# Kernel tuning notes

Hardware: AMD Instinct MI355X
Metric: run time of the kernel (lower is better)

## Reference

```python
import jax, jax.numpy as jnp
import numpy as np

HIDDEN = 1024
N_HEADS = 16
HEAD_DIM = HIDDEN // N_HEADS
MAX_DIST = 50
B, S = 2, 2048


def setup_inputs() -> dict:
    key = jax.random.key(0)
    ks = jax.random.split(key, 12)
    s = 1.0 / np.sqrt(HIDDEN)
    return {
        "hidden_states": jax.random.normal(ks[0], (B, S, HIDDEN), dtype=jnp.float32),
        "dist_matrix": jax.random.randint(ks[1], (B, S, S), 0, 60, dtype=jnp.int32),
        "idf_scores": jax.random.uniform(ks[2], (B, S), dtype=jnp.float32),
        "attention_mask": jnp.ones((B, S), dtype=jnp.int32),
        "Wq": jax.random.normal(ks[3], (HIDDEN, HIDDEN), dtype=jnp.float32) * s,
        "bq": jnp.zeros((HIDDEN,), dtype=jnp.float32),
        "Wk": jax.random.normal(ks[4], (HIDDEN, HIDDEN), dtype=jnp.float32) * s,
        "bk": jnp.zeros((HIDDEN,), dtype=jnp.float32),
        "Wv": jax.random.normal(ks[5], (HIDDEN, HIDDEN), dtype=jnp.float32) * s,
        "bv": jnp.zeros((HIDDEN,), dtype=jnp.float32),
        "Wo": jax.random.normal(ks[6], (HIDDEN, HIDDEN), dtype=jnp.float32) * s,
        "bo": jnp.zeros((HIDDEN,), dtype=jnp.float32),
        "struct_emb": jax.random.normal(ks[7], (MAX_DIST + 1, N_HEADS), dtype=jnp.float32) * 0.02,
        "rarity_weight": jnp.full((1,), 0.1, dtype=jnp.float32),
    }


def reference(hidden_states, dist_matrix, idf_scores, attention_mask,
              Wq, bq, Wk, bk, Wv, bv, Wo, bo, struct_emb, rarity_weight):
    b, s, _ = hidden_states.shape
    scale = 1.0 / np.sqrt(HEAD_DIM)

    def split_heads(x):  # [b,s,H] -> [b,h,s,d]
        return x.reshape(b, s, N_HEADS, HEAD_DIM).transpose(0, 2, 1, 3)

    Q = split_heads(hidden_states @ Wq.T + bq)
    K = split_heads(hidden_states @ Wk.T + bk)
    V = split_heads(hidden_states @ Wv.T + bv)

    scores = jnp.einsum('bhqd,bhkd->bhqk', Q, K) * scale

    # structural bias: gather per-head bias by clamped pairwise distance
    dist_c = jnp.clip(dist_matrix, 0, MAX_DIST)
    scores = scores + struct_emb[dist_c].transpose(0, 3, 1, 2)  # [b,h,q,k]

    # rarity bias: idf_i broadcasts over keys, idf_j over queries (as in torch code)
    rarity = rarity_weight[0] * (idf_scores[:, None, None, :] + idf_scores[:, None, :, None])
    scores = scores + rarity

    # mask: [b,1,1,s] over key axis
    mask = attention_mask[:, None, None, :]
    scores = jnp.where(mask == 0, -jnp.inf, scores)

    attn = jax.nn.softmax(scores, axis=-1)
    out = jnp.einsum('bhqk,bhkd->bhqd', attn, V)
    out = out.transpose(0, 2, 1, 3).reshape(b, s, HIDDEN)
    out = out @ Wo.T + bo
    return out, attn
```

## Files before the change

### kernel.cpp

```cpp
#include <hip/hip_runtime.h>
#include <math.h>

#define S 2048
#define HID 1024
#define NH 16
#define HD 64
#define BH 32

typedef __attribute__((ext_vector_type(8))) short bf16x8;
typedef __attribute__((ext_vector_type(4))) float f32x4;
typedef __attribute__((ext_vector_type(8))) unsigned short ush8;
typedef unsigned short u16;

__device__ __forceinline__ u16 f2bf(float f) {
    unsigned u = __float_as_uint(f);
    u += 0x7fffu + ((u >> 16) & 1u);
    return (u16)(u >> 16);
}
__device__ __forceinline__ float bf2f(u16 h) {
    return __uint_as_float(((unsigned)h) << 16);
}

__global__ __launch_bounds__(256)
void split_all(const float* __restrict__ X,  const float* __restrict__ Wq,
               const float* __restrict__ Wk, const float* __restrict__ Wv,
               const float* __restrict__ Wo,
               u16* __restrict__ Xh,  u16* __restrict__ Xl,
               u16* __restrict__ Wqh, u16* __restrict__ Wql,
               u16* __restrict__ Wkh, u16* __restrict__ Wkl,
               u16* __restrict__ Wvh, u16* __restrict__ Wvl,
               u16* __restrict__ Woh, u16* __restrict__ Wol)
{
    size_t i = (size_t)blockIdx.x * 256 + threadIdx.x;
    const float* s; u16* h; u16* l; size_t o;
    if (i < (size_t)(1u << 20)) { s = X; h = Xh; l = Xl; o = i; }
    else {
        size_t j = i - (1u << 20);
        int wsel = (int)(j >> 18); o = j & ((1u << 18) - 1);
        s = wsel == 0 ? Wq  : wsel == 1 ? Wk  : wsel == 2 ? Wv  : Wo;
        h = wsel == 0 ? Wqh : wsel == 1 ? Wkh : wsel == 2 ? Wvh : Woh;
        l = wsel == 0 ? Wql : wsel == 1 ? Wkl : wsel == 2 ? Wvl : Wol;
    }
    float4 v = ((const float4*)s)[o];
    ushort4 hv, lv;
#define SP(c, k) { unsigned u = __float_as_uint(v.c);                      \
                   unsigned hb = u & 0xffff0000u;                          \
                   float d = v.c - __uint_as_float(hb);                    \
                   hv.k = (u16)(u >> 16);                                  \
                   lv.k = (u16)(__float_as_uint(d) >> 16); }
    SP(x, x) SP(y, y) SP(z, z) SP(w, w)
#undef SP
    ((ushort4*)h)[o] = hv;
    ((ushort4*)l)[o] = lv;
}

__global__ __launch_bounds__(256)
void qkv_mfma(const u16* __restrict__ Xh, const u16* __restrict__ Xl,
              const u16* __restrict__ Wh_q, const u16* __restrict__ Wl_q,
              const u16* __restrict__ Wh_k, const u16* __restrict__ Wl_k,
              const u16* __restrict__ Wh_v, const u16* __restrict__ Wl_v,
              const float* __restrict__ bq_, const float* __restrict__ bk_,
              const float* __restrict__ bv_,
              u16* __restrict__ Qb, u16* __restrict__ Kb, u16* __restrict__ Vb)
{
    const int z = blockIdx.z;
    const u16* __restrict__ Wh = z == 0 ? Wh_q : (z == 1 ? Wh_k : Wh_v);
    const u16* __restrict__ Wl = z == 0 ? Wl_q : (z == 1 ? Wl_k : Wl_v);
    const float* __restrict__ bias = z == 0 ? bq_ : (z == 1 ? bk_ : bv_);
    u16* __restrict__ Ob = z == 0 ? Qb : (z == 1 ? Kb : Vb);

    __shared__ u16 Ah[128 * 40], Al[128 * 40], Bh[128 * 40], Bl[128 * 40];
    const int t = threadIdx.x;
    const int m0 = blockIdx.y * 128, n0 = blockIdx.x * 128;
    const int srow = t >> 1, scol = (t & 1) * 16;
    const int lane = t & 63, w = t >> 6, wm = w >> 1, wn = w & 1;
    const int lr = lane & 15, lg = lane >> 4;

    f32x4 acc[4][4] = {{{0.f, 0.f, 0.f, 0.f}}};
    for (int k0 = 0; k0 < HID; k0 += 32) {
        size_t ao = (size_t)(m0 + srow) * HID + k0 + scol;
        size_t bo = (size_t)(n0 + srow) * HID + k0 + scol;
        ush8 a0 = *(const ush8*)(Xh + ao), a1 = *(const ush8*)(Xh + ao + 8);
        ush8 a2 = *(const ush8*)(Xl + ao), a3 = *(const ush8*)(Xl + ao + 8);
        ush8 b0 = *(const ush8*)(Wh + bo), b1 = *(const ush8*)(Wh + bo + 8);
        ush8 b2 = *(const ush8*)(Wl + bo), b3 = *(const ush8*)(Wl + bo + 8);
        __syncthreads();
        *(ush8*)&Ah[srow * 40 + scol] = a0; *(ush8*)&Ah[srow * 40 + scol + 8] = a1;
        *(ush8*)&Al[srow * 40 + scol] = a2; *(ush8*)&Al[srow * 40 + scol + 8] = a3;
        *(ush8*)&Bh[srow * 40 + scol] = b0; *(ush8*)&Bh[srow * 40 + scol + 8] = b1;
        *(ush8*)&Bl[srow * 40 + scol] = b2; *(ush8*)&Bl[srow * 40 + scol + 8] = b3;
        __syncthreads();
        bf16x8 fbh[4], fbl[4];
#pragma unroll
        for (int ni = 0; ni < 4; ++ni) {
            fbh[ni] = *(const bf16x8*)&Bh[(wn * 64 + ni * 16 + lr) * 40 + lg * 8];
            fbl[ni] = *(const bf16x8*)&Bl[(wn * 64 + ni * 16 + lr) * 40 + lg * 8];
        }
#pragma unroll
        for (int mi = 0; mi < 4; ++mi) {
            bf16x8 fah = *(const bf16x8*)&Ah[(wm * 64 + mi * 16 + lr) * 40 + lg * 8];
            bf16x8 fal = *(const bf16x8*)&Al[(wm * 64 + mi * 16 + lr) * 40 + lg * 8];
#pragma unroll
            for (int ni = 0; ni < 4; ++ni) {
                f32x4 c = acc[mi][ni];
                c = __builtin_amdgcn_mfma_f32_16x16x32_bf16(fah, fbh[ni], c, 0, 0, 0);
                c = __builtin_amdgcn_mfma_f32_16x16x32_bf16(fah, fbl[ni], c, 0, 0, 0);
                c = __builtin_amdgcn_mfma_f32_16x16x32_bf16(fal, fbh[ni], c, 0, 0, 0);
                acc[mi][ni] = c;
            }
        }
    }
    const int hh = blockIdx.x * 2 + wn;
    float bv4[4];
#pragma unroll
    for (int ni = 0; ni < 4; ++ni) bv4[ni] = bias[n0 + wn * 64 + ni * 16 + lr];
#pragma unroll
    for (int mi = 0; mi < 4; ++mi)
#pragma unroll
        for (int r = 0; r < 4; ++r) {
            int m = m0 + wm * 64 + mi * 16 + lg * 4 + r;
            int b = m >> 11, s = m & 2047;
#pragma unroll
            for (int ni = 0; ni < 4; ++ni) {
                float v = acc[mi][ni][r] + bv4[ni];
                Ob[((size_t)(b * NH + hh) * S + s) * HD + ni * 16 + lr] = f2bf(v);
            }
        }
}

__global__ __launch_bounds__(256)
void out_mfma(const u16* __restrict__ Xh, const u16* __restrict__ Xl,
              const u16* __restrict__ Wh, const u16* __restrict__ Wl,
              const float* __restrict__ bo_, float* __restrict__ Y)
{
    __shared__ u16 Ah[128 * 40], Al[128 * 40], Bh[128 * 40], Bl[128 * 40];
    const int t = threadIdx.x;
    const int m0 = blockIdx.y * 128, n0 = blockIdx.x * 128;
    const int srow = t >> 1, scol = (t & 1) * 16;
    const int lane = t & 63, w = t >> 6, wm = w >> 1, wn = w & 1;
    const int lr = lane & 15, lg = lane >> 4;

    f32x4 acc[4][4] = {{{0.f, 0.f, 0.f, 0.f}}};
    for (int k0 = 0; k0 < HID; k0 += 32) {
        size_t ao = (size_t)(m0 + srow) * HID + k0 + scol;
        size_t bo = (size_t)(n0 + srow) * HID + k0 + scol;
        ush8 a0 = *(const ush8*)(Xh + ao), a1 = *(const ush8*)(Xh + ao + 8);
        ush8 a2 = *(const ush8*)(Xl + ao), a3 = *(const ush8*)(Xl + ao + 8);
        ush8 b0 = *(const ush8*)(Wh + bo), b1 = *(const ush8*)(Wh + bo + 8);
        ush8 b2 = *(const ush8*)(Wl + bo), b3 = *(const ush8*)(Wl + bo + 8);
        __syncthreads();
        *(ush8*)&Ah[srow * 40 + scol] = a0; *(ush8*)&Ah[srow * 40 + scol + 8] = a1;
        *(ush8*)&Al[srow * 40 + scol] = a2; *(ush8*)&Al[srow * 40 + scol + 8] = a3;
        *(ush8*)&Bh[srow * 40 + scol] = b0; *(ush8*)&Bh[srow * 40 + scol + 8] = b1;
        *(ush8*)&Bl[srow * 40 + scol] = b2; *(ush8*)&Bl[srow * 40 + scol + 8] = b3;
        __syncthreads();
        bf16x8 fbh[4], fbl[4];
#pragma unroll
        for (int ni = 0; ni < 4; ++ni) {
            fbh[ni] = *(const bf16x8*)&Bh[(wn * 64 + ni * 16 + lr) * 40 + lg * 8];
            fbl[ni] = *(const bf16x8*)&Bl[(wn * 64 + ni * 16 + lr) * 40 + lg * 8];
        }
#pragma unroll
        for (int mi = 0; mi < 4; ++mi) {
            bf16x8 fah = *(const bf16x8*)&Ah[(wm * 64 + mi * 16 + lr) * 40 + lg * 8];
            bf16x8 fal = *(const bf16x8*)&Al[(wm * 64 + mi * 16 + lr) * 40 + lg * 8];
#pragma unroll
            for (int ni = 0; ni < 4; ++ni) {
                f32x4 c = acc[mi][ni];
                c = __builtin_amdgcn_mfma_f32_16x16x32_bf16(fah, fbh[ni], c, 0, 0, 0);
                c = __builtin_amdgcn_mfma_f32_16x16x32_bf16(fah, fbl[ni], c, 0, 0, 0);
                c = __builtin_amdgcn_mfma_f32_16x16x32_bf16(fal, fbh[ni], c, 0, 0, 0);
                acc[mi][ni] = c;
            }
        }
    }
    float bv4[4];
#pragma unroll
    for (int ni = 0; ni < 4; ++ni) bv4[ni] = bo_[n0 + wn * 64 + ni * 16 + lr];
#pragma unroll
    for (int mi = 0; mi < 4; ++mi)
#pragma unroll
        for (int r = 0; r < 4; ++r) {
            int m = m0 + wm * 64 + mi * 16 + lg * 4 + r;
#pragma unroll
            for (int ni = 0; ni < 4; ++ni)
                Y[(size_t)m * HID + n0 + wn * 64 + ni * 16 + lr] =
                    acc[mi][ni][r] + bv4[ni];
        }
}

__global__ __launch_bounds__(512)
void attn_pv(const u16* __restrict__ Qb, const u16* __restrict__ Kb,
             const u16* __restrict__ Vb,
             const int* __restrict__ dist, const float* __restrict__ idf,
             const int* __restrict__ amask, const float* __restrict__ semb,
             const float* __restrict__ rw,
             float* __restrict__ attn, u16* __restrict__ OHh, u16* __restrict__ OHl)
{
    __shared__ u16 QPs[128 * 72];
    __shared__ u16 Ks[64 * 72];
    __shared__ u16 Vts[64 * 72];
    __shared__ float SeH[51];

    const int n = blockIdx.x;
    const int xcd = n & 7, rest = n >> 3;
    const int h = rest & 15;
    const int pair = xcd * 4 + (rest >> 4);
    const int b = pair >> 4, qt = pair & 15;
    const int bh = b * NH + h, q0 = qt * 128;

    const int t = threadIdx.x, lane = t & 63, w = t >> 6;
    const int lr = lane & 15, lg = lane >> 4;

    if (t < 51) SeH[t] = semb[t * NH + h];
    {
        int r = t >> 2, c = (t & 3) * 16;
        const u16* qrow = Qb + ((size_t)bh * S + q0 + r) * HD + c;
        *(ush8*)&QPs[r * 72 + c]     = *(const ush8*)qrow;
        *(ush8*)&QPs[r * 72 + c + 8] = *(const ush8*)(qrow + 8);
    }
    __syncthreads();

    bf16x8 qa0 = *(const bf16x8*)&QPs[(w * 16 + lr) * 72 + lg * 8];
    bf16x8 qa1 = *(const bf16x8*)&QPs[(w * 16 + lr) * 72 + 32 + lg * 8];

    const float rwv = rw[0];
    float idqv[4];
#pragma unroll
    for (int r = 0; r < 4; ++r)
        idqv[r] = idf[b * S + q0 + w * 16 + lg * 4 + r];

    float M[4]    = {-INFINITY, -INFINITY, -INFINITY, -INFINITY};
    float Ssum[4] = {0.f, 0.f, 0.f, 0.f};

    for (int k0 = 0; k0 < S; k0 += 64) {
        __syncthreads();
        *(ush8*)&Ks[(t >> 3) * 72 + (t & 7) * 8] =
            *(const ush8*)(Kb + ((size_t)bh * S + k0 + (t >> 3)) * HD + (t & 7) * 8);
        __syncthreads();

        f32x4 c4[4];
#pragma unroll
        for (int ni = 0; ni < 4; ++ni) {
            bf16x8 kf0 = *(const bf16x8*)&Ks[(ni * 16 + lr) * 72 + lg * 8];
            bf16x8 kf1 = *(const bf16x8*)&Ks[(ni * 16 + lr) * 72 + 32 + lg * 8];
            f32x4 c = {0.f, 0.f, 0.f, 0.f};
            c = __builtin_amdgcn_mfma_f32_16x16x32_bf16(qa0, kf0, c, 0, 0, 0);
            c = __builtin_amdgcn_mfma_f32_16x16x32_bf16(qa1, kf1, c, 0, 0, 0);
            c4[ni] = c;
        }

        float idk[4]; int mk[4];
#pragma unroll
        for (int ni = 0; ni < 4; ++ni) {
            int k = k0 + ni * 16 + lr;
            idk[ni] = idf[b * S + k];
            mk[ni]  = amask[b * S + k];
        }
#pragma unroll
        for (int r = 0; r < 4; ++r) {
            const int q = q0 + w * 16 + lg * 4 + r;
            const int* drow = dist + ((size_t)b * S + q) * S + k0;
            float sc[4];
#pragma unroll
            for (int ni = 0; ni < 4; ++ni) {
                int dc = drow[ni * 16 + lr];
                dc = dc < 0 ? 0 : (dc > 50 ? 50 : dc);
                float v = c4[ni][r] * 0.125f + SeH[dc] + rwv * (idqv[r] + idk[ni]);
                if (mk[ni] == 0) v = -INFINITY;
                sc[ni] = v;
            }
            float m = fmaxf(fmaxf(sc[0], sc[1]), fmaxf(sc[2], sc[3]));
#pragma unroll
            for (int off = 1; off < 16; off <<= 1) m = fmaxf(m, __shfl_xor(m, off));
            if (m > -INFINITY) {
                float s = 0.f;
#pragma unroll
                for (int ni = 0; ni < 4; ++ni) s += __expf(sc[ni] - m);
#pragma unroll
                for (int off = 1; off < 16; off <<= 1) s += __shfl_xor(s, off);
                if (m > M[r]) {
                    Ssum[r] = Ssum[r] * __expf(M[r] - m) + s;
                    M[r] = m;
                } else {
                    Ssum[r] += s * __expf(m - M[r]);
                }
            }
        }
    }
    float Iv[4];
#pragma unroll
    for (int r = 0; r < 4; ++r) Iv[r] = 1.0f / Ssum[r];

    f32x4 oacc[4] = {{0.f, 0.f, 0.f, 0.f}};

    for (int k0 = 0; k0 < S; k0 += 64) {
        __syncthreads();
        *(ush8*)&Ks[(t >> 3) * 72 + (t & 7) * 8] =
            *(const ush8*)(Kb + ((size_t)bh * S + k0 + (t >> 3)) * HD + (t & 7) * 8);
        {
            ush8 v0 = *(const ush8*)(Vb + ((size_t)bh * S + k0 + lane) * HD + w * 8);
#pragma unroll
            for (int j = 0; j < 8; ++j)
                Vts[(w * 8 + j) * 72 + lane] = ((const u16*)&v0)[j];
        }
        __syncthreads();

        f32x4 c4[4];
#pragma unroll
        for (int ni = 0; ni < 4; ++ni) {
            bf16x8 kf0 = *(const bf16x8*)&Ks[(ni * 16 + lr) * 72 + lg * 8];
            bf16x8 kf1 = *(const bf16x8*)&Ks[(ni * 16 + lr) * 72 + 32 + lg * 8];
            f32x4 c = {0.f, 0.f, 0.f, 0.f};
            c = __builtin_amdgcn_mfma_f32_16x16x32_bf16(qa0, kf0, c, 0, 0, 0);
            c = __builtin_amdgcn_mfma_f32_16x16x32_bf16(qa1, kf1, c, 0, 0, 0);
            c4[ni] = c;
        }

        float idk[4]; int mk[4];
#pragma unroll
        for (int ni = 0; ni < 4; ++ni) {
            int k = k0 + ni * 16 + lr;
            idk[ni] = idf[b * S + k];
            mk[ni]  = amask[b * S + k];
        }
#pragma unroll
        for (int r = 0; r < 4; ++r) {
            const int q = q0 + w * 16 + lg * 4 + r;
            const int* drow = dist + ((size_t)b * S + q) * S + k0;
            float* arow = attn + ((size_t)bh * S + q) * S + k0;
#pragma unroll
            for (int ni = 0; ni < 4; ++ni) {
                int dc = drow[ni * 16 + lr];
                dc = dc < 0 ? 0 : (dc > 50 ? 50 : dc);
                float sv = c4[ni][r] * 0.125f + SeH[dc] + rwv * (idqv[r] + idk[ni]);
                if (mk[ni] == 0) sv = -INFINITY;
                float p = __expf(sv - M[r]) * Iv[r];
                arow[ni * 16 + lr] = p;
                QPs[(w * 16 + lg * 4 + r) * 72 + ni * 16 + lr] = f2bf(p);
            }
        }
        bf16x8 pa0 = *(const bf16x8*)&QPs[(w * 16 + lr) * 72 + lg * 8];
        bf16x8 pa1 = *(const bf16x8*)&QPs[(w * 16 + lr) * 72 + 32 + lg * 8];
#pragma unroll
        for (int ni = 0; ni < 4; ++ni) {
            bf16x8 vb0 = *(const bf16x8*)&Vts[(ni * 16 + lr) * 72 + lg * 8];
            bf16x8 vb1 = *(const bf16x8*)&Vts[(ni * 16 + lr) * 72 + 32 + lg * 8];
            oacc[ni] = __builtin_amdgcn_mfma_f32_16x16x32_bf16(pa0, vb0, oacc[ni], 0, 0, 0);
            oacc[ni] = __builtin_amdgcn_mfma_f32_16x16x32_bf16(pa1, vb1, oacc[ni], 0, 0, 0);
        }
    }

#pragma unroll
    for (int r = 0; r < 4; ++r) {
        const int q = q0 + w * 16 + lg * 4 + r;
#pragma unroll
        for (int ni = 0; ni < 4; ++ni) {
            float v = oacc[ni][r];
            u16 hi = f2bf(v);
            u16 lo = f2bf(v - bf2f(hi));
            size_t off = ((size_t)b * S + q) * HID + h * HD + ni * 16 + lr;
            OHh[off] = hi;
            OHl[off] = lo;
        }
    }
}

extern "C" void kernel_launch(void* const* d_in, const int* in_sizes, int n_in,
                              void* d_out, int out_size, void* d_ws, size_t ws_size,
                              hipStream_t stream)
{
    const float* hs   = (const float*)d_in[0];
    const int*   dist = (const int*)d_in[1];
    const float* idf  = (const float*)d_in[2];
    const int*   am   = (const int*)d_in[3];
    const float* Wq   = (const float*)d_in[4];
    const float* bq   = (const float*)d_in[5];
    const float* Wk   = (const float*)d_in[6];
    const float* bk   = (const float*)d_in[7];
    const float* Wv   = (const float*)d_in[8];
    const float* bv   = (const float*)d_in[9];
    const float* Wo   = (const float*)d_in[10];
    const float* bo   = (const float*)d_in[11];
    const float* se   = (const float*)d_in[12];
    const float* rw   = (const float*)d_in[13];

    float* out  = (float*)d_out;
    float* attn = out + (size_t)2 * S * HID;

    u16* Xh = (u16*)attn;
    u16* Xl = Xh + (size_t)4096 * 1024;

    u16* Qb  = (u16*)d_ws;
    u16* Kb  = Qb  + (size_t)BH * S * HD;
    u16* Vb  = Kb  + (size_t)BH * S * HD;
    u16* OHh = Vb  + (size_t)BH * S * HD;
    u16* OHl = OHh + (size_t)4096 * 1024;
    u16* Woh = OHl + (size_t)4096 * 1024;
    u16* Wol = Woh + (size_t)1024 * 1024;
    u16* Wqh = Wol + (size_t)1024 * 1024;
    u16* Wql = Wqh + (size_t)1024 * 1024;
    u16* Wkh = Wql + (size_t)1024 * 1024;
    u16* Wkl = Wkh + (size_t)1024 * 1024;
    u16* Wvh = Wkl + (size_t)1024 * 1024;
    u16* Wvl = Wvh + (size_t)1024 * 1024;

    dim3 blk(256);
    split_all<<<dim3(8192), blk, 0, stream>>>(hs, Wq, Wk, Wv, Wo,
                                              Xh, Xl, Wqh, Wql, Wkh, Wkl,
                                              Wvh, Wvl, Woh, Wol);
    qkv_mfma<<<dim3(8, 32, 3), blk, 0, stream>>>(Xh, Xl, Wqh, Wql, Wkh, Wkl,
                                                 Wvh, Wvl, bq, bk, bv, Qb, Kb, Vb);
    attn_pv<<<dim3(512), dim3(512), 0, stream>>>(Qb, Kb, Vb, dist, idf, am, se, rw,
                                                 attn, OHh, OHl);
    out_mfma<<<dim3(8, 32), blk, 0, stream>>>(OHh, OHl, Woh, Wol, bo, out);
}
```

Measured before the change: 486.4 us.

## Split attention key range across warp halves with transposed S tile and vector I/O

Restructures the attention kernel into 64-query tiles with 8 warps, where two warp groups each process half the key range, doubling the grid to 1024 blocks. The score tile is computed transposed (K as A operand), so each lane owns one query row and reads dist/idf/mask and writes attn with 16-byte vector accesses instead of scattered scalar ones. Per-row max/sum now accumulate per lane, are merged across lanes by shuffles and across the two key halves through shared memory, and partial PV outputs are reduced in LDS at the end. It also adds setprio around MFMA and a launch-bounds occupancy hint, at the cost of extra sync and reduction steps.

```diff
diff --git a/kernel.cpp b/kernel.cpp
--- a/kernel.cpp
+++ b/kernel.cpp
@@ -11,6 +11,7 @@
 typedef __attribute__((ext_vector_type(4))) float f32x4;
 typedef __attribute__((ext_vector_type(8))) unsigned short ush8;
 typedef unsigned short u16;
+typedef unsigned int u32;
 
 __device__ __forceinline__ u16 f2bf(float f) {
     unsigned u = __float_as_uint(f);
@@ -189,7 +190,7 @@
         }
 }
 
-__global__ __launch_bounds__(512)
+__global__ __launch_bounds__(512, 8)
 void attn_pv(const u16* __restrict__ Qb, const u16* __restrict__ Kb,
              const u16* __restrict__ Vb,
              const int* __restrict__ dist, const float* __restrict__ idf,
@@ -197,172 +198,202 @@
              const float* __restrict__ rw,
              float* __restrict__ attn, u16* __restrict__ OHh, u16* __restrict__ OHl)
 {
-    __shared__ u16 QPs[128 * 72];
-    __shared__ u16 Ks[64 * 72];
-    __shared__ u16 Vts[64 * 72];
+    __shared__ u16 Ps[128 * 72];
+    __shared__ u16 Ks[2][32 * 72];
+    __shared__ u16 Vts[2][64 * 40];
     __shared__ float SeH[51];
+    __shared__ float MSm[128], MSs[128];
 
     const int n = blockIdx.x;
     const int xcd = n & 7, rest = n >> 3;
     const int h = rest & 15;
-    const int pair = xcd * 4 + (rest >> 4);
-    const int b = pair >> 4, qt = pair & 15;
-    const int bh = b * NH + h, q0 = qt * 128;
+    const int pair = xcd * 8 + (rest >> 4);
+    const int b = pair >> 5, qt = pair & 31;
+    const int bh = b * NH + h, q0 = qt * 64;
 
     const int t = threadIdx.x, lane = t & 63, w = t >> 6;
+    const int wq = w & 3, wk = w >> 2;
     const int lr = lane & 15, lg = lane >> 4;
+    const int q = q0 + wq * 16 + lr;
 
     if (t < 51) SeH[t] = semb[t * NH + h];
     {
-        int r = t >> 2, c = (t & 3) * 16;
-        const u16* qrow = Qb + ((size_t)bh * S + q0 + r) * HD + c;
-        *(ush8*)&QPs[r * 72 + c]     = *(const ush8*)qrow;
-        *(ush8*)&QPs[r * 72 + c + 8] = *(const ush8*)(qrow + 8);
+        int r = t >> 3, c = (t & 7) * 8;
+        *(ush8*)&Ps[r * 72 + c] = *(const ush8*)(Qb + ((size_t)bh * S + q0 + r) * HD + c);
     }
     __syncthreads();
 
-    bf16x8 qa0 = *(const bf16x8*)&QPs[(w * 16 + lr) * 72 + lg * 8];
-    bf16x8 qa1 = *(const bf16x8*)&QPs[(w * 16 + lr) * 72 + 32 + lg * 8];
+    bf16x8 qa0 = *(const bf16x8*)&Ps[(wq * 16 + lr) * 72 + lg * 8];
+    bf16x8 qa1 = *(const bf16x8*)&Ps[(wq * 16 + lr) * 72 + 32 + lg * 8];
 
     const float rwv = rw[0];
-    float idqv[4];
-#pragma unroll
-    for (int r = 0; r < 4; ++r)
-        idqv[r] = idf[b * S + q0 + w * 16 + lg * 4 + r];
-
-    float M[4]    = {-INFINITY, -INFINITY, -INFINITY, -INFINITY};
-    float Ssum[4] = {0.f, 0.f, 0.f, 0.f};
-
-    for (int k0 = 0; k0 < S; k0 += 64) {
-        __syncthreads();
-        *(ush8*)&Ks[(t >> 3) * 72 + (t & 7) * 8] =
-            *(const ush8*)(Kb + ((size_t)bh * S + k0 + (t >> 3)) * HD + (t & 7) * 8);
-        __syncthreads();
-
-        f32x4 c4[4];
+    const float idq = idf[b * S + q];
+    const int* dptr = dist + (size_t)(b * S + q) * S;
+    const size_t kbase = (size_t)bh * S;
+    const int srow = (t & 255) >> 3, scol = (t & 7) * 8, shalf = t >> 8;
+    const int vr = (t & 255) & 31, vd = ((t & 255) >> 5) * 8;
+
+    float M = -INFINITY, Ssum = 0.f;
+
+    for (int it = 0; it < 32; ++it) {
+        const int k0  = wk * 1024 + it * 32;
+        const int k0s = shalf * 1024 + it * 32;
+        __syncthreads();
+        *(ush8*)&Ks[shalf][srow * 72 + scol] =
+            *(const ush8*)(Kb + (kbase + k0s + srow) * HD + scol);
+        __syncthreads();
+
+        f32x4 c2[2];
+        __builtin_amdgcn_s_setprio(1);
+#pragma unroll
+        for (int ni = 0; ni < 2; ++ni) {
+            bf16x8 kf0 = *(const bf16x8*)&Ks[wk][(ni * 16 + lr) * 72 + lg * 8];
+            bf16x8 kf1 = *(const bf16x8*)&Ks[wk][(ni * 16 + lr) * 72 + 32 + lg * 8];
+            f32x4 c = {0.f, 0.f, 0.f, 0.f};
+            c = __builtin_amdgcn_mfma_f32_16x16x32_bf16(kf0, qa0, c, 0, 0, 0);
+            c = __builtin_amdgcn_mfma_f32_16x16x32_bf16(kf1, qa1, c, 0, 0, 0);
+            c2[ni] = c;
+        }
+        __builtin_amdgcn_s_setprio(0);
+
+        float sc[2][4];
+        float chm = -INFINITY;
+#pragma unroll
+        for (int ni = 0; ni < 2; ++ni) {
+            const int kb = k0 + ni * 16 + lg * 4;
+            int4   dv = *(const int4*)(dptr + kb);
+            float4 ik = *(const float4*)(idf + b * S + kb);
+            int4   mv = *(const int4*)(amask + b * S + kb);
+            int   dd[4] = {dv.x, dv.y, dv.z, dv.w};
+            float ikf[4] = {ik.x, ik.y, ik.z, ik.w};
+            int   mm[4] = {mv.x, mv.y, mv.z, mv.w};
+#pragma unroll
+            for (int r = 0; r < 4; ++r) {
+                int dc = dd[r]; dc = dc < 0 ? 0 : (dc > 50 ? 50 : dc);
+                float v = c2[ni][r] * 0.125f + SeH[dc] + rwv * (idq + ikf[r]);
+                if (mm[r] == 0) v = -INFINITY;
+                sc[ni][r] = v;
+                chm = fmaxf(chm, v);
+            }
+        }
+        if (chm > -INFINITY) {
+            float mn = fmaxf(M, chm);
+            float s = 0.f;
+#pragma unroll
+            for (int ni = 0; ni < 2; ++ni)
+#pragma unroll
+                for (int r = 0; r < 4; ++r) s += __expf(sc[ni][r] - mn);
+            Ssum = Ssum * __expf(M - mn) + s;
+            M = mn;
+        }
+    }
+#pragma unroll
+    for (int off = 16; off <= 32; off <<= 1) {
+        float Mo = __shfl_xor(M, off), So = __shfl_xor(Ssum, off);
+        float mn = fmaxf(M, Mo);
+        Ssum = Ssum * __expf(M - mn) + So * __expf(Mo - mn);
+        M = mn;
+    }
+    if (lg == 0) { MSm[w * 16 + lr] = M; MSs[w * 16 + lr] = Ssum; }
+    __syncthreads();
+    {
+        int pw = (w + 4) & 7;
+        float Mo = MSm[pw * 16 + lr], So = MSs[pw * 16 + lr];
+        float mn = fmaxf(M, Mo);
+        Ssum = Ssum * __expf(M - mn) + So * __expf(Mo - mn);
+        M = mn;
+    }
+    const float Iv = 1.0f / Ssum;
+
+    float* aptr = attn + (kbase + q) * S;
+    f32x4 oacc[4] = {{0.f,0.f,0.f,0.f},{0.f,0.f,0.f,0.f},
+                     {0.f,0.f,0.f,0.f},{0.f,0.f,0.f,0.f}};
+
+    for (int it = 0; it < 32; ++it) {
+        const int k0  = wk * 1024 + it * 32;
+        const int k0s = shalf * 1024 + it * 32;
+        __syncthreads();
+        *(ush8*)&Ks[shalf][srow * 72 + scol] =
+            *(const ush8*)(Kb + (kbase + k0s + srow) * HD + scol);
+        {
+            ush8 v0 = *(const ush8*)(Vb + (kbase + k0s + vr) * HD + vd);
+#pragma unroll
+            for (int j = 0; j < 8; ++j)
+                Vts[shalf][(vd + j) * 40 + vr] = v0[j];
+        }
+        __syncthreads();
+
+        f32x4 c2[2];
+        __builtin_amdgcn_s_setprio(1);
+#pragma unroll
+        for (int ni = 0; ni < 2; ++ni) {
+            bf16x8 kf0 = *(const bf16x8*)&Ks[wk][(ni * 16 + lr) * 72 + lg * 8];
+            bf16x8 kf1 = *(const bf16x8*)&Ks[wk][(ni * 16 + lr) * 72 + 32 + lg * 8];
+            f32x4 c = {0.f, 0.f, 0.f, 0.f};
+            c = __builtin_amdgcn_mfma_f32_16x16x32_bf16(kf0, qa0, c, 0, 0, 0);
+            c = __builtin_amdgcn_mfma_f32_16x16x32_bf16(kf1, qa1, c, 0, 0, 0);
+            c2[ni] = c;
+        }
+        __builtin_amdgcn_s_setprio(0);
+
+#pragma unroll
+        for (int ni = 0; ni < 2; ++ni) {
+            const int kb = k0 + ni * 16 + lg * 4;
+            int4   dv = *(const int4*)(dptr + kb);
+            float4 ik = *(const float4*)(idf + b * S + kb);
+            int4   mv = *(const int4*)(amask + b * S + kb);
+            int   dd[4] = {dv.x, dv.y, dv.z, dv.w};
+            float ikf[4] = {ik.x, ik.y, ik.z, ik.w};
+            int   mm[4] = {mv.x, mv.y, mv.z, mv.w};
+            float pp[4];
+#pragma unroll
+            for (int r = 0; r < 4; ++r) {
+                int dc = dd[r]; dc = dc < 0 ? 0 : (dc > 50 ? 50 : dc);
+                float v = c2[ni][r] * 0.125f + SeH[dc] + rwv * (idq + ikf[r]);
+                if (mm[r] == 0) v = -INFINITY;
+                pp[r] = __expf(v - M) * Iv;
+            }
+            float4 st = make_float4(pp[0], pp[1], pp[2], pp[3]);
+            *(float4*)(aptr + kb) = st;
+            uint2 pk;
+            pk.x = (u32)f2bf(pp[0]) | ((u32)f2bf(pp[1]) << 16);
+            pk.y = (u32)f2bf(pp[2]) | ((u32)f2bf(pp[3]) << 16);
+            *(uint2*)&Ps[(w * 16 + lr) * 72 + ni * 16 + lg * 4] = pk;
+        }
+        bf16x8 pa = *(const bf16x8*)&Ps[(w * 16 + lr) * 72 + lg * 8];
+        __builtin_amdgcn_s_setprio(1);
 #pragma unroll
         for (int ni = 0; ni < 4; ++ni) {
-            bf16x8 kf0 = *(const bf16x8*)&Ks[(ni * 16 + lr) * 72 + lg * 8];
-            bf16x8 kf1 = *(const bf16x8*)&Ks[(ni * 16 + lr) * 72 + 32 + lg * 8];
-            f32x4 c = {0.f, 0.f, 0.f, 0.f};
-            c = __builtin_amdgcn_mfma_f32_16x16x32_bf16(qa0, kf0, c, 0, 0, 0);
-            c = __builtin_amdgcn_mfma_f32_16x16x32_bf16(qa1, kf1, c, 0, 0, 0);
-            c4[ni] = c;
-        }
-
-        float idk[4]; int mk[4];
-#pragma unroll
-        for (int ni = 0; ni < 4; ++ni) {
-            int k = k0 + ni * 16 + lr;
-            idk[ni] = idf[b * S + k];
-            mk[ni]  = amask[b * S + k];
-        }
-#pragma unroll
-        for (int r = 0; r < 4; ++r) {
-            const int q = q0 + w * 16 + lg * 4 + r;
-            const int* drow = dist + ((size_t)b * S + q) * S + k0;
-            float sc[4];
-#pragma unroll
-            for (int ni = 0; ni < 4; ++ni) {
-                int dc = drow[ni * 16 + lr];
-                dc = dc < 0 ? 0 : (dc > 50 ? 50 : dc);
-                float v = c4[ni][r] * 0.125f + SeH[dc] + rwv * (idqv[r] + idk[ni]);
-                if (mk[ni] == 0) v = -INFINITY;
-                sc[ni] = v;
-            }
-            float m = fmaxf(fmaxf(sc[0], sc[1]), fmaxf(sc[2], sc[3]));
-#pragma unroll
-            for (int off = 1; off < 16; off <<= 1) m = fmaxf(m, __shfl_xor(m, off));
-            if (m > -INFINITY) {
-                float s = 0.f;
-#pragma unroll
-                for (int ni = 0; ni < 4; ++ni) s += __expf(sc[ni] - m);
-#pragma unroll
-                for (int off = 1; off < 16; off <<= 1) s += __shfl_xor(s, off);
-                if (m > M[r]) {
-                    Ssum[r] = Ssum[r] * __expf(M[r] - m) + s;
-                    M[r] = m;
-                } else {
-                    Ssum[r] += s * __expf(m - M[r]);
-                }
-            }
-        }
-    }
-    float Iv[4];
-#pragma unroll
-    for (int r = 0; r < 4; ++r) Iv[r] = 1.0f / Ssum[r];
-
-    f32x4 oacc[4] = {{0.f, 0.f, 0.f, 0.f}};
-
-    for (int k0 = 0; k0 < S; k0 += 64) {
-        __syncthreads();
-        *(ush8*)&Ks[(t >> 3) * 72 + (t & 7) * 8] =
-            *(const ush8*)(Kb + ((size_t)bh * S + k0 + (t >> 3)) * HD + (t & 7) * 8);
-        {
-            ush8 v0 = *(const ush8*)(Vb + ((size_t)bh * S + k0 + lane) * HD + w * 8);
-#pragma unroll
-            for (int j = 0; j < 8; ++j)
-                Vts[(w * 8 + j) * 72 + lane] = ((const u16*)&v0)[j];
-        }
-        __syncthreads();
-
-        f32x4 c4[4];
-#pragma unroll
-        for (int ni = 0; ni < 4; ++ni) {
-            bf16x8 kf0 = *(const bf16x8*)&Ks[(ni * 16 + lr) * 72 + lg * 8];
-            bf16x8 kf1 = *(const bf16x8*)&Ks[(ni * 16 + lr) * 72 + 32 + lg * 8];
-            f32x4 c = {0.f, 0.f, 0.f, 0.f};
-            c = __builtin_amdgcn_mfma_f32_16x16x32_bf16(qa0, kf0, c, 0, 0, 0);
-            c = __builtin_amdgcn_mfma_f32_16x16x32_bf16(qa1, kf1, c, 0, 0, 0);
-            c4[ni] = c;
-        }
-
-        float idk[4]; int mk[4];
-#pragma unroll
-        for (int ni = 0; ni < 4; ++ni) {
-            int k = k0 + ni * 16 + lr;
-            idk[ni] = idf[b * S + k];
-            mk[ni]  = amask[b * S + k];
-        }
-#pragma unroll
-        for (int r = 0; r < 4; ++r) {
-            const int q = q0 + w * 16 + lg * 4 + r;
-            const int* drow = dist + ((size_t)b * S + q) * S + k0;
-            float* arow = attn + ((size_t)bh * S + q) * S + k0;
-#pragma unroll
-            for (int ni = 0; ni < 4; ++ni) {
-                int dc = drow[ni * 16 + lr];
-                dc = dc < 0 ? 0 : (dc > 50 ? 50 : dc);
-                float sv = c4[ni][r] * 0.125f + SeH[dc] + rwv * (idqv[r] + idk[ni]);
-                if (mk[ni] == 0) sv = -INFINITY;
-                float p = __expf(sv - M[r]) * Iv[r];
-                arow[ni * 16 + lr] = p;
-                QPs[(w * 16 + lg * 4 + r) * 72 + ni * 16 + lr] = f2bf(p);
-            }
-        }
-        bf16x8 pa0 = *(const bf16x8*)&QPs[(w * 16 + lr) * 72 + lg * 8];
-        bf16x8 pa1 = *(const bf16x8*)&QPs[(w * 16 + lr) * 72 + 32 + lg * 8];
-#pragma unroll
-        for (int ni = 0; ni < 4; ++ni) {
-            bf16x8 vb0 = *(const bf16x8*)&Vts[(ni * 16 + lr) * 72 + lg * 8];
-            bf16x8 vb1 = *(const bf16x8*)&Vts[(ni * 16 + lr) * 72 + 32 + lg * 8];
-            oacc[ni] = __builtin_amdgcn_mfma_f32_16x16x32_bf16(pa0, vb0, oacc[ni], 0, 0, 0);
-            oacc[ni] = __builtin_amdgcn_mfma_f32_16x16x32_bf16(pa1, vb1, oacc[ni], 0, 0, 0);
-        }
-    }
-
-#pragma unroll
-    for (int r = 0; r < 4; ++r) {
-        const int q = q0 + w * 16 + lg * 4 + r;
-#pragma unroll
-        for (int ni = 0; ni < 4; ++ni) {
-            float v = oacc[ni][r];
-            u16 hi = f2bf(v);
-            u16 lo = f2bf(v - bf2f(hi));
-            size_t off = ((size_t)b * S + q) * HID + h * HD + ni * 16 + lr;
-            OHh[off] = hi;
-            OHl[off] = lo;
-        }
+            bf16x8 vb = *(const bf16x8*)&Vts[wk][(ni * 16 + lr) * 40 + lg * 8];
+            oacc[ni] = __builtin_amdgcn_mfma_f32_16x16x32_bf16(pa, vb, oacc[ni], 0, 0, 0);
+        }
+        __builtin_amdgcn_s_setprio(0);
+    }
+
+    __syncthreads();
+    if (wk == 1) {
+        float* OA = (float*)Ps;
+#pragma unroll
+        for (int ni = 0; ni < 4; ++ni)
+#pragma unroll
+            for (int r = 0; r < 4; ++r)
+                OA[(wq * 16 + lg * 4 + r) * 64 + ni * 16 + lr] = oacc[ni][r];
+    }
+    __syncthreads();
+    if (wk == 0) {
+        const float* OA = (const float*)Ps;
+#pragma unroll
+        for (int ni = 0; ni < 4; ++ni)
+#pragma unroll
+            for (int r = 0; r < 4; ++r) {
+                float v = oacc[ni][r] + OA[(wq * 16 + lg * 4 + r) * 64 + ni * 16 + lr];
+                u16 hi = f2bf(v);
+                u16 lo = f2bf(v - bf2f(hi));
+                int qq = q0 + wq * 16 + lg * 4 + r;
+                size_t off = ((size_t)b * S + qq) * HID + h * HD + ni * 16 + lr;
+                OHh[off] = hi;
+                OHl[off] = lo;
+            }
     }
 }
 
@@ -411,7 +442,7 @@
                                               Wvh, Wvl, Woh, Wol);
     qkv_mfma<<<dim3(8, 32, 3), blk, 0, stream>>>(Xh, Xl, Wqh, Wql, Wkh, Wkl,
                                                  Wvh, Wvl, bq, bk, bv, Qb, Kb, Vb);
-    attn_pv<<<dim3(512), dim3(512), 0, stream>>>(Qb, Kb, Vb, dist, idf, am, se, rw,
-                                                 attn, OHh, OHl);
+    attn_pv<<<dim3(1024), dim3(512), 0, stream>>>(Qb, Kb, Vb, dist, idf, am, se, rw,
+                                                  attn, OHh, OHl);
     out_mfma<<<dim3(8, 32), blk, 0, stream>>>(OHh, OHl, Woh, Wol, bo, out);
 }
```

Result: slower. 627.5 us (+29.0%).
